# Performance work log

Measured on AMD Instinct MI355X. Metric: run time of the kernel, lower is better.

## Reference

```python
import jax, jax.numpy as jnp
import numpy as np

NUM_PATCHES = 64
PATCH_DIM = 256
HIDDEN = 512
HEADS = 8
SEQ = 1 + NUM_PATCHES  # 65
OUT_DIM = 10
BLOCKS = 6


def _ln2d(x, w, b):
    # LayerNorm over last two dims (seq, hidden), eps=1e-5, affine shape (SEQ, HIDDEN)
    mu = jnp.mean(x, axis=(-2, -1), keepdims=True)
    var = jnp.var(x, axis=(-2, -1), keepdims=True)
    return (x - mu) / jnp.sqrt(var + 1e-5) * w + b


def setup_inputs() -> dict:
    key = jax.random.key(0)
    ks = jax.random.split(key, 22)
    s = 0.02
    inp = {
        'X': jax.random.normal(ks[0], (256, 1, 128, 128), jnp.float32),
        'Wp': jax.random.normal(ks[1], (PATCH_DIM, HIDDEN), jnp.float32) * s,
        'bp': jnp.zeros((HIDDEN,), jnp.float32),
        'cls': jax.random.uniform(ks[2], (1, HIDDEN), jnp.float32),
        'pos': jax.random.uniform(ks[3], (SEQ, HIDDEN), jnp.float32),
        'ln1_w': jnp.ones((SEQ, HIDDEN), jnp.float32),
        'ln1_b': jnp.zeros((SEQ, HIDDEN), jnp.float32),
        'Wq': jax.random.normal(ks[4], (HEADS, HIDDEN, HIDDEN), jnp.float32) * s,
        'bq': jnp.zeros((HEADS, HIDDEN), jnp.float32),
        'Wk': jax.random.normal(ks[5], (HEADS, HIDDEN, HIDDEN), jnp.float32) * s,
        'bk': jnp.zeros((HEADS, HIDDEN), jnp.float32),
        'Wv': jax.random.normal(ks[6], (HEADS, HIDDEN, HIDDEN), jnp.float32) * s,
        'bv': jnp.zeros((HEADS, HIDDEN), jnp.float32),
        'Wo': jax.random.normal(ks[7], (HEADS * HIDDEN, HIDDEN), jnp.float32) * s,
        'bo': jnp.zeros((HIDDEN,), jnp.float32),
        'ln2_w': jnp.ones((SEQ, HIDDEN), jnp.float32),
        'ln2_b': jnp.zeros((SEQ, HIDDEN), jnp.float32),
        'W2': jax.random.normal(ks[8], (HIDDEN, HIDDEN), jnp.float32) * s,
        'b2': jnp.zeros((HIDDEN,), jnp.float32),
        'Wh': jax.random.normal(ks[9], (HIDDEN, OUT_DIM), jnp.float32) * s,
        'bh': jnp.zeros((OUT_DIM,), jnp.float32),
    }
    return inp


def reference(X, Wp, bp, cls, pos, ln1_w, ln1_b, Wq, bq, Wk, bk, Wv, bv, Wo, bo, ln2_w, ln2_b, W2, b2, Wh, bh):
    N = X.shape[0]
    patches = X.reshape(N, NUM_PATCHES, PATCH_DIM)
    E = patches @ Wp + bp                              # [N, 64, 512]
    E = jnp.concatenate([jnp.broadcast_to(cls, (N, 1, HIDDEN)), E], axis=1)
    Z = E + pos                                        # [N, 65, 512]
    scale = 1.0 / float(HIDDEN) ** 2                   # note: /hidden_dim**2 as in source
    for _ in range(BLOCKS):  # SAME weights reused each block (shared modules)
        Zn = _ln2d(Z, ln1_w, ln1_b)
        q = jnp.einsum('nsd,hde->nhse', Zn, Wq) + bq[None, :, None, :]
        k = jnp.einsum('nsd,hde->nhse', Zn, Wk) + bk[None, :, None, :]
        v = jnp.einsum('nsd,hde->nhse', Zn, Wv) + bv[None, :, None, :]
        attn = jax.nn.softmax(jnp.einsum('nhse,nhte->nhst', q, k) * scale, axis=-1)
        h = jnp.einsum('nhst,nhte->nhse', attn, v)     # [N, H, S, D]
        Hcat = jnp.transpose(h, (0, 2, 1, 3)).reshape(N, SEQ, HEADS * HIDDEN)
        res1 = Hcat @ Wo + bo                          # [N, 65, 512]
        Z = _ln2d(res1 + Z, ln2_w, ln2_b) @ W2 + b2    # no residual after this (as in source)
    return jnp.tanh(Z[:, 0] @ Wh + bh)
```

## Files before the change

kernel.cpp:

```cpp
#include <hip/hip_runtime.h>


typedef unsigned short u16;
typedef __attribute__((ext_vector_type(8))) short s8v;
typedef __attribute__((ext_vector_type(4))) float f4v;

#define MFMA16(a, b, c) __builtin_amdgcn_mfma_f32_16x16x32_bf16((a), (b), (c), 0, 0, 0)

__device__ __forceinline__ u16 f2bf(float f) {
    union { float f; unsigned int u; } c; c.f = f;
    unsigned int u = c.u;
    return (u16)((u + 0x7FFFu + ((u >> 16) & 1u)) >> 16);
}
__device__ __forceinline__ unsigned int pack2(float a, float b) {
    return (unsigned int)f2bf(a) | ((unsigned int)f2bf(b) << 16);
}
__device__ __forceinline__ float bflo(unsigned int u) {
    union { unsigned int i; float f; } c; c.i = u << 16; return c.f;
}
__device__ __forceinline__ float bfhi(unsigned int u) {
    union { unsigned int i; float f; } c; c.i = u & 0xffff0000u; return c.f;
}

__global__ __launch_bounds__(256) void vit_prep1(
    const float* __restrict__ Wp, const float* __restrict__ W2,
    const float* __restrict__ Wo, const float* __restrict__ Wv,
    const float* __restrict__ w1, const float* __restrict__ b1,
    const float* __restrict__ ln2w, const float* __restrict__ ln2b,
    const float* __restrict__ bv,
    u16* __restrict__ WpT, u16* __restrict__ W2T, u16* __restrict__ WoT,
    u16* __restrict__ Ap, float* __restrict__ W1c, float* __restrict__ B1m,
    unsigned int* __restrict__ w1q, unsigned int* __restrict__ w1t,
    unsigned int* __restrict__ lnp, float* __restrict__ bep) {
    __shared__ float t[64][65];
    const int bid = blockIdx.x, tid = threadIdx.x;
    if (bid < 608) {
        const float* in; u16* out; int R, C, bx, by;
        if (bid < 32)      { in = Wp; out = WpT; R = 256;  C = 512; int l = bid;      bx = l & 3;  by = l >> 2; }
        else if (bid < 96) { in = W2; out = W2T; R = 512;  C = 512; int l = bid - 32; bx = l & 7;  by = l >> 3; }
        else               { in = Wo; out = WoT; R = 4096; C = 512; int l = bid - 96; bx = l & 63; by = l >> 6; }
        const int r0 = bx * 64, c0 = by * 64;
        const int lr = tid >> 6, lc = tid & 63;
#pragma unroll
        for (int i = 0; i < 16; ++i) {
            int rr = i * 4 + lr;
            t[rr][lc] = in[(long)(r0 + rr) * C + c0 + lc];
        }
        __syncthreads();
#pragma unroll
        for (int i = 0; i < 16; ++i) {
            int rr = i * 4 + lr;
            out[(long)(c0 + rr) * R + r0 + lc] = f2bf(t[lc][rr]);
        }
    } else if (bid < 1632) {
        int base = (bid - 608) * 2048 + tid;
#pragma unroll
        for (int q = 0; q < 8; ++q) {
            int o = base + q * 256;
            int d = o >> 12, he = o & 4095;
            int h = he >> 9, e = he & 511;
            Ap[o] = f2bf(Wv[((long)h << 18) + (d << 9) + e]);
        }
    } else if (bid < 1830) {
        int id = (bid - 1632) * 256 + tid;
        if (id < 512) {
            float sw = 0.f, sb = 0.f;
            for (int s = 0; s < 65; ++s) { sw += w1[s * 512 + id]; sb += b1[s * 512 + id]; }
            W1c[id] = sw; B1m[id] = sb * (1.f / 65.f);
        }
        int i1 = id - 512;
        if (i1 >= 0 && i1 < 16896) {
            int s2 = i1 >> 9, d = i1 & 511;
            float lo = w1[(2 * s2) * 512 + d];
            float hi = (2 * s2 + 1 < 65) ? w1[(2 * s2 + 1) * 512 + d] : 0.f;
            unsigned int pk = pack2(lo, hi);
            if (s2 < 32) w1q[(s2 >> 2) * 2048 + d * 4 + (s2 & 3)] = pk;
            else         w1t[d] = pk;
        }
        int i2 = id - 17408;
        if (i2 >= 0 && i2 < 33280) {
            lnp[i2] = ((unsigned int)f2bf(ln2w[i2]) << 16) | (unsigned int)f2bf(ln2b[i2]);
        }
    } else {
        int z = bid - 1830;
#pragma unroll
        for (int jj = 0; jj < 2; ++jj) {
            int j = tid + jj * 256;
            float a = 0.f;
            for (int he = z * 32; he < z * 32 + 32; ++he)
                a += bv[he] * Wo[(long)he * 512 + j];
            bep[z * 512 + j] = a;
        }
    }
}

__global__ __launch_bounds__(512) void vit_prep2(
    const float* __restrict__ Wpart, const float* __restrict__ bep,
    const float* __restrict__ bo, unsigned int* __restrict__ Weffp,
    float* __restrict__ beff) {
    const int bid = blockIdx.x, tid = threadIdx.x;
    if (bid < 256) {
        int id = bid * 512 + tid;
        int kk = id >> 9, j = id & 511;
        float lo = 0.f, hi = 0.f;
#pragma unroll 4
        for (int z = 0; z < 32; ++z) {
            lo += Wpart[(long)z * 262144 + (2 * kk) * 512 + j];
            hi += Wpart[(long)z * 262144 + (2 * kk + 1) * 512 + j];
        }
        Weffp[(kk >> 2) * 2048 + j * 4 + (kk & 3)] = pack2(lo, hi);
    } else {
        float a = bo[tid];
        for (int z = 0; z < 128; ++z) a += bep[z * 512 + tid];
        beff[tid] = a;
    }
}

template<int K>
__global__ __launch_bounds__(512) void vit_gemmB(
    const u16* __restrict__ A, const u16* __restrict__ BT,
    float* __restrict__ out, int Arow, int Brow) {
    constexpr int BROW = K + 8;
    __shared__ __align__(16) u16 Bs[128 * BROW];
    const int tid = threadIdx.x, w = tid >> 6, lane = tid & 63;
    const int ml = lane & 15, kh = lane >> 4;
    const int m0 = blockIdx.x * 256, n0 = blockIdx.y * 128, k0 = blockIdx.z * K;
    out += (long)blockIdx.z * 262144;

    constexpr int CH = K / 8;
    for (int idx = tid; idx < 128 * CH; idx += 512) {
        int r = idx / CH, c = idx - r * CH;
        *(uint4*)&Bs[r * BROW + c * 8] =
            *(const uint4*)(BT + (long)(n0 + r) * Brow + k0 + c * 8);
    }
    __syncthreads();

    const u16* Abase = A + (long)(m0 + w * 32 + ml) * Arow + k0 + kh * 8;
    const long Astep16 = (long)16 * Arow;

    f4v acc[2][8];
#pragma unroll
    for (int mt = 0; mt < 2; ++mt)
#pragma unroll
        for (int j = 0; j < 8; ++j) acc[mt][j] = (f4v){0.f, 0.f, 0.f, 0.f};

    constexpr int NSTEP = K / 32;
    s8v a_cur[2], a_nxt[2];
    a_cur[0] = *(const s8v*)(Abase);
    a_cur[1] = *(const s8v*)(Abase + Astep16);
#pragma unroll
    for (int s = 0; s < NSTEP; ++s) {
        if (s + 1 < NSTEP) {
            a_nxt[0] = *(const s8v*)(Abase + (s + 1) * 32);
            a_nxt[1] = *(const s8v*)(Abase + Astep16 + (s + 1) * 32);
        }
#pragma unroll
        for (int j = 0; j < 8; ++j) {
            s8v b = *(const s8v*)&Bs[(j * 16 + ml) * BROW + s * 32 + kh * 8];
            acc[0][j] = MFMA16(a_cur[0], b, acc[0][j]);
            acc[1][j] = MFMA16(a_cur[1], b, acc[1][j]);
        }
        a_cur[0] = a_nxt[0]; a_cur[1] = a_nxt[1];
    }

#pragma unroll
    for (int mt = 0; mt < 2; ++mt)
#pragma unroll
        for (int j = 0; j < 8; ++j) {
            int n_g = n0 + j * 16 + ml;
#pragma unroll
            for (int r = 0; r < 4; ++r) {
                int m_g = m0 + w * 32 + mt * 16 + kh * 4 + r;
                out[(long)m_g * 512 + n_g] = acc[mt][j][r];
            }
        }
}

__global__ __launch_bounds__(512) void vit_fused(
    const float* __restrict__ X, const u16* __restrict__ WpT,
    const float* __restrict__ bp, const float* __restrict__ cls,
    const float* __restrict__ pos,
    const float* __restrict__ W1c, const float* __restrict__ B1m,
    const unsigned int* __restrict__ w1q, const unsigned int* __restrict__ w1t,
    const unsigned int* __restrict__ Weffp, const float* __restrict__ beff,
    const unsigned int* __restrict__ lnp,
    const u16* __restrict__ W2T, const float* __restrict__ b2,
    const float* __restrict__ Wh, const float* __restrict__ bh,
    float* __restrict__ out) {
    __shared__ __align__(16) char blob[139392];
    float* ZL   = (float*)blob;
    float* RmL  = (float*)(blob + 133120);
    float* ZnmL = (float*)(blob + 135168);
    float* csL  = (float*)(blob + 137216);
    float* red  = (float*)(blob + 139264);
    const float4* Rm4 = (const float4*)RmL;

    const int n = blockIdx.x, tid = threadIdx.x;
    const int w = tid >> 6, lane = tid & 63;
    const int ml = lane & 15, kh = lane >> 4;

    {
        const float* xf = X + (long)n * 16384;
        f4v eacc[4][4];
#pragma unroll
        for (int mt = 0; mt < 4; ++mt)
#pragma unroll
            for (int j = 0; j < 4; ++j) eacc[mt][j] = (f4v){0.f, 0.f, 0.f, 0.f};
#pragma unroll 1
        for (int st = 0; st < 8; ++st) {
            s8v b[4];
#pragma unroll
            for (int j = 0; j < 4; ++j)
                b[j] = *(const s8v*)(WpT + (long)(w * 64 + j * 16 + ml) * 256 +
                                     st * 32 + kh * 8);
#pragma unroll
            for (int mt = 0; mt < 4; ++mt) {
                const float* ap = xf + (mt * 16 + ml) * 256 + st * 32 + kh * 8;
                float4 xa = *(const float4*)ap;
                float4 xb = *(const float4*)(ap + 4);
                union { s8v v; u16 h[8]; } au;
                au.h[0] = f2bf(xa.x); au.h[1] = f2bf(xa.y);
                au.h[2] = f2bf(xa.z); au.h[3] = f2bf(xa.w);
                au.h[4] = f2bf(xb.x); au.h[5] = f2bf(xb.y);
                au.h[6] = f2bf(xb.z); au.h[7] = f2bf(xb.w);
#pragma unroll
                for (int j = 0; j < 4; ++j) eacc[mt][j] = MFMA16(au.v, b[j], eacc[mt][j]);
            }
        }
        float se = 0.f, sse = 0.f;
        float v0 = cls[tid] + pos[tid];
        ZL[tid] = v0; se += v0; sse += v0 * v0;
#pragma unroll
        for (int mt = 0; mt < 4; ++mt)
#pragma unroll
            for (int j = 0; j < 4; ++j) {
                int col = w * 64 + j * 16 + ml;
                float bpv = bp[col];
#pragma unroll
                for (int r = 0; r < 4; ++r) {
                    int zrow = mt * 16 + kh * 4 + r + 1;
                    float v = eacc[mt][j][r] + bpv + pos[zrow * 512 + col];
                    ZL[zrow * 512 + col] = v;
                    se += v; sse += v * v;
                }
            }
        for (int off = 32; off > 0; off >>= 1) {
            se += __shfl_down(se, off); sse += __shfl_down(sse, off);
        }
        if (lane == 0) { red[w] = se; red[8 + w] = sse; }
    }
    __syncthreads();

#pragma unroll 1
    for (int blk = 0; blk < 6; ++blk) {
        float S = 0.f, SS = 0.f;
#pragma unroll
        for (int i = 0; i < 8; ++i) { S += red[i]; SS += red[8 + i]; }
        const float mu = S * (1.f / 33280.f);
        const float r1 = rsqrtf(SS * (1.f / 33280.f) - mu * mu + 1e-5f);

        {
            float sw = 0.f, cs = 0.f;
            const uint4* W1Q = (const uint4*)w1q;
#pragma unroll 2
            for (int g = 0; g < 8; ++g) {
                uint4 u = W1Q[g * 512 + tid];
                int s0 = g * 8;
                float z0 = ZL[(s0 + 0) * 512 + tid], z1 = ZL[(s0 + 1) * 512 + tid];
                float z2 = ZL[(s0 + 2) * 512 + tid], z3 = ZL[(s0 + 3) * 512 + tid];
                float z4 = ZL[(s0 + 4) * 512 + tid], z5 = ZL[(s0 + 5) * 512 + tid];
                float z6 = ZL[(s0 + 6) * 512 + tid], z7 = ZL[(s0 + 7) * 512 + tid];
                cs += z0 + z1 + z2 + z3 + z4 + z5 + z6 + z7;
                sw += z0 * bflo(u.x) + z1 * bfhi(u.x);
                sw += z2 * bflo(u.y) + z3 * bfhi(u.y);
                sw += z4 * bflo(u.z) + z5 * bfhi(u.z);
                sw += z6 * bflo(u.w) + z7 * bfhi(u.w);
            }
            float zt = ZL[64 * 512 + tid];
            cs += zt;
            sw += zt * bflo(w1t[tid]);
            ZnmL[tid] = r1 * ((sw - mu * W1c[tid]) * (1.f / 65.f)) + B1m[tid];
            csL[tid] = cs;
        }
        __syncthreads();

        float mu2, r2;
        {
            const uint4* W4 = (const uint4*)Weffp;
            float a0 = 0.f, a1 = 0.f, a2 = 0.f, a3 = 0.f;
#pragma unroll 4
            for (int g = 0; g < 64; ++g) {
                uint4 u = W4[g * 512 + tid];
                int k0 = g * 8;
                a0 += ZnmL[k0 + 0] * bflo(u.x) + ZnmL[k0 + 1] * bfhi(u.x);
                a1 += ZnmL[k0 + 2] * bflo(u.y) + ZnmL[k0 + 3] * bfhi(u.y);
                a2 += ZnmL[k0 + 4] * bflo(u.z) + ZnmL[k0 + 5] * bfhi(u.z);
                a3 += ZnmL[k0 + 6] * bflo(u.w) + ZnmL[k0 + 7] * bfhi(u.w);
            }
            float rm = a0 + a1 + a2 + a3 + beff[tid];
            RmL[tid] = rm;
            float p1 = rm, p2 = rm * rm, p3 = rm * csL[tid];
            for (int off = 32; off > 0; off >>= 1) {
                p1 += __shfl_down(p1, off);
                p2 += __shfl_down(p2, off);
                p3 += __shfl_down(p3, off);
            }
            if (lane == 0) { red[w] = p1; red[8 + w] = p2; red[16 + w] = p3; }
            __syncthreads();
            float SR = 0.f, SR2 = 0.f, SRC = 0.f;
#pragma unroll
            for (int i = 0; i < 8; ++i) {
                SR += red[i]; SR2 += red[8 + i]; SRC += red[16 + i];
            }
            float S2 = S + 65.f * SR;
            float SS2 = SS + 2.f * SRC + 65.f * SR2;
            mu2 = S2 * (1.f / 33280.f);
            r2 = rsqrtf(SS2 * (1.f / 33280.f) - mu2 * mu2 + 1e-5f);
        }

#pragma unroll 1
        for (int it = 0; it < 9; ++it) {
            int row = it * 8 + w;
            if (row < 65) {
                const float* zr = ZL + row * 512;
                float4 z0 = *(const float4*)(zr + lane * 8);
                float4 z1 = *(const float4*)(zr + lane * 8 + 4);
                uint4 l0 = *(const uint4*)(lnp + row * 512 + lane * 8);
                uint4 l1 = *(const uint4*)(lnp + row * 512 + lane * 8 + 4);
                float4 rm0 = Rm4[lane * 2], rm1 = Rm4[lane * 2 + 1];
                float o0 = ((z0.x + rm0.x) - mu2) * r2 * bfhi(l0.x) + bflo(l0.x);
                float o1 = ((z0.y + rm0.y) - mu2) * r2 * bfhi(l0.y) + bflo(l0.y);
                float o2 = ((z0.z + rm0.z) - mu2) * r2 * bfhi(l0.z) + bflo(l0.z);
                float o3 = ((z0.w + rm0.w) - mu2) * r2 * bfhi(l0.w) + bflo(l0.w);
                float o4 = ((z1.x + rm1.x) - mu2) * r2 * bfhi(l1.x) + bflo(l1.x);
                float o5 = ((z1.y + rm1.y) - mu2) * r2 * bfhi(l1.y) + bflo(l1.y);
                float o6 = ((z1.z + rm1.z) - mu2) * r2 * bfhi(l1.z) + bflo(l1.z);
                float o7 = ((z1.w + rm1.w) - mu2) * r2 * bfhi(l1.w) + bflo(l1.w);
                uint4 pk;
                pk.x = pack2(o0, o1); pk.y = pack2(o2, o3);
                pk.z = pack2(o4, o5); pk.w = pack2(o6, o7);
                *(uint4*)(blob + row * 2064 + lane * 16) = pk;
            }
        }
        __syncthreads();

        int arow[5];
#pragma unroll
        for (int mt = 0; mt < 5; ++mt) {
            int rr = mt * 16 + ml;
            arow[mt] = (rr > 64) ? 64 : rr;
        }
        f4v acc[5][4];
#pragma unroll
        for (int mt = 0; mt < 5; ++mt)
#pragma unroll
            for (int j = 0; j < 4; ++j) acc[mt][j] = (f4v){0.f, 0.f, 0.f, 0.f};
        {
            s8v bcur[4], bnxt[4];
#pragma unroll
            for (int j = 0; j < 4; ++j)
                bcur[j] = *(const s8v*)(W2T + (long)(w * 64 + j * 16 + ml) * 512 + kh * 8);
#pragma unroll 1
            for (int st = 0; st < 16; ++st) {
                if (st < 15) {
#pragma unroll
                    for (int j = 0; j < 4; ++j)
                        bnxt[j] = *(const s8v*)(W2T + (long)(w * 64 + j * 16 + ml) * 512 +
                                                (st + 1) * 32 + kh * 8);
                }
#pragma unroll
                for (int mt = 0; mt < 5; ++mt) {
                    s8v a = *(const s8v*)(blob + arow[mt] * 2064 + st * 64 + kh * 16);
#pragma unroll
                    for (int j = 0; j < 4; ++j) acc[mt][j] = MFMA16(a, bcur[j], acc[mt][j]);
                }
#pragma unroll
                for (int j = 0; j < 4; ++j) bcur[j] = bnxt[j];
            }
        }
        __syncthreads();

        if (blk < 5) {
            float sn = 0.f, ssn = 0.f;
#pragma unroll
            for (int mt = 0; mt < 5; ++mt)
#pragma unroll
                for (int j = 0; j < 4; ++j) {
                    int col = w * 64 + j * 16 + ml;
                    float bbv = b2[col];
#pragma unroll
                    for (int r = 0; r < 4; ++r) {
                        int row = mt * 16 + kh * 4 + r;
                        if (row < 65) {
                            float v = acc[mt][j][r] + bbv;
                            ZL[row * 512 + col] = v;
                            sn += v; ssn += v * v;
                        }
                    }
                }
            for (int off = 32; off > 0; off >>= 1) {
                sn += __shfl_down(sn, off); ssn += __shfl_down(ssn, off);
            }
            if (lane == 0) { red[w] = sn; red[8 + w] = ssn; }
            __syncthreads();
        } else {
            if (kh == 0) {
#pragma unroll
                for (int j = 0; j < 4; ++j) {
                    int col = w * 64 + j * 16 + ml;
                    RmL[col] = acc[0][j][0] + b2[col];
                }
            }
            __syncthreads();
            if (tid < 64) {
                float a10[10];
#pragma unroll
                for (int jj = 0; jj < 10; ++jj) a10[jj] = 0.f;
#pragma unroll
                for (int i = 0; i < 8; ++i) {
                    int k = tid * 8 + i;
                    float zv = RmL[k];
#pragma unroll
                    for (int jj = 0; jj < 10; ++jj) a10[jj] += zv * Wh[k * 10 + jj];
                }
                for (int off = 32; off > 0; off >>= 1) {
#pragma unroll
                    for (int jj = 0; jj < 10; ++jj) a10[jj] += __shfl_down(a10[jj], off);
                }
                if (tid == 0) {
#pragma unroll
                    for (int jj = 0; jj < 10; ++jj)
                        out[n * 10 + jj] = tanhf(a10[jj] + bh[jj]);
                }
            }
        }
    }
}

static const size_t OFF_WPT   = 0;
static const size_t OFF_W2T   = 262144;
static const size_t OFF_WOT   = 786432;
static const size_t OFF_AP    = 4980736;
static const size_t OFF_WEFFP = 9175040;
static const size_t OFF_WPART = 9699328;
static const size_t OFF_BEP   = 43253760;
static const size_t OFF_BEFF  = 43515904;
static const size_t OFF_W1C   = 43517952;
static const size_t OFF_B1M   = 43520000;
static const size_t OFF_W1Q   = 43522048;
static const size_t OFF_W1T   = 43587584;
static const size_t OFF_LNP   = 43589632;

extern "C" void kernel_launch(void* const* d_in, const int* in_sizes, int n_in,
                              void* d_out, int out_size, void* d_ws, size_t ws_size,
                              hipStream_t stream) {
    const float* X    = (const float*)d_in[0];
    const float* Wp   = (const float*)d_in[1];
    const float* bp   = (const float*)d_in[2];
    const float* cls  = (const float*)d_in[3];
    const float* pos  = (const float*)d_in[4];
    const float* ln1w = (const float*)d_in[5];
    const float* ln1b = (const float*)d_in[6];
    const float* Wv   = (const float*)d_in[11];
    const float* bv   = (const float*)d_in[12];
    const float* Wo   = (const float*)d_in[13];
    const float* bo   = (const float*)d_in[14];
    const float* ln2w = (const float*)d_in[15];
    const float* ln2b = (const float*)d_in[16];
    const float* W2   = (const float*)d_in[17];
    const float* b2   = (const float*)d_in[18];
    const float* Wh   = (const float*)d_in[19];
    const float* bh   = (const float*)d_in[20];

    char* ws = (char*)d_ws;
    u16* WpT     = (u16*)(ws + OFF_WPT);
    u16* W2T     = (u16*)(ws + OFF_W2T);
    u16* WoT     = (u16*)(ws + OFF_WOT);
    u16* Ap      = (u16*)(ws + OFF_AP);
    unsigned int* Weffp = (unsigned int*)(ws + OFF_WEFFP);
    float* Wpart = (float*)(ws + OFF_WPART);
    float* bep   = (float*)(ws + OFF_BEP);
    float* beff  = (float*)(ws + OFF_BEFF);
    float* W1c   = (float*)(ws + OFF_W1C);
    float* B1m   = (float*)(ws + OFF_B1M);
    unsigned int* w1q = (unsigned int*)(ws + OFF_W1Q);
    unsigned int* w1t = (unsigned int*)(ws + OFF_W1T);
    unsigned int* lnp = (unsigned int*)(ws + OFF_LNP);

    vit_prep1<<<dim3(1958), dim3(256), 0, stream>>>(
        Wp, W2, Wo, Wv, ln1w, ln1b, ln2w, ln2b, bv,
        WpT, W2T, WoT, Ap, W1c, B1m, w1q, w1t, lnp, bep);
    vit_gemmB<128><<<dim3(2, 4, 32), dim3(512), 0, stream>>>(
        Ap, WoT, Wpart, 4096, 4096);
    vit_prep2<<<dim3(257), dim3(512), 0, stream>>>(Wpart, bep, bo, Weffp, beff);

    vit_fused<<<dim3(256), dim3(512), 0, stream>>>(
        X, WpT, bp, cls, pos, W1c, B1m, w1q, w1t, Weffp, beff, lnp, W2T, b2,
        Wh, bh, (float*)d_out);
}
```

Measured before the change: 333.3 us.

## Double fused kernel block to 1024 threads and split reductions across halves

The fused ViT kernel now launches 1024 threads per block instead of 512. The column-sum and Weff matvec stages split their reduction dimension between two thread halves and combine partials through new shared buffers, and the MFMA GEMMs give each wave 32 columns instead of 64. The aim is more waves per CU to hide latency in this one-block-per-sample kernel, since only 256 blocks run. In exchange it adds extra syncthreads and partial-sum passes, grows shared memory use, and tightens the register budget under launch_bounds(1024).

```diff
diff --git a/kernel.cpp b/kernel.cpp
--- a/kernel.cpp
+++ b/kernel.cpp
@@ -176,7 +176,7 @@
         }
 }
 
-__global__ __launch_bounds__(512) void vit_fused(
+__global__ __launch_bounds__(1024) void vit_fused(
     const float* __restrict__ X, const u16* __restrict__ WpT,
     const float* __restrict__ bp, const float* __restrict__ cls,
     const float* __restrict__ pos,
@@ -187,31 +187,33 @@
     const u16* __restrict__ W2T, const float* __restrict__ b2,
     const float* __restrict__ Wh, const float* __restrict__ bh,
     float* __restrict__ out) {
-    __shared__ __align__(16) char blob[139392];
+    __shared__ __align__(16) char blob[145600];
     float* ZL   = (float*)blob;
     float* RmL  = (float*)(blob + 133120);
     float* ZnmL = (float*)(blob + 135168);
-    float* csL  = (float*)(blob + 137216);
-    float* red  = (float*)(blob + 139264);
+    float* swP  = (float*)(blob + 137216);
+    float* csP  = (float*)(blob + 141312);
+    float* red  = (float*)(blob + 145408);
     const float4* Rm4 = (const float4*)RmL;
 
     const int n = blockIdx.x, tid = threadIdx.x;
     const int w = tid >> 6, lane = tid & 63;
     const int ml = lane & 15, kh = lane >> 4;
+    const int j0 = w * 32;
 
     {
         const float* xf = X + (long)n * 16384;
-        f4v eacc[4][4];
+        f4v eacc[4][2];
 #pragma unroll
         for (int mt = 0; mt < 4; ++mt)
 #pragma unroll
-            for (int j = 0; j < 4; ++j) eacc[mt][j] = (f4v){0.f, 0.f, 0.f, 0.f};
+            for (int j = 0; j < 2; ++j) eacc[mt][j] = (f4v){0.f, 0.f, 0.f, 0.f};
 #pragma unroll 1
         for (int st = 0; st < 8; ++st) {
-            s8v b[4];
-#pragma unroll
-            for (int j = 0; j < 4; ++j)
-                b[j] = *(const s8v*)(WpT + (long)(w * 64 + j * 16 + ml) * 256 +
+            s8v b[2];
+#pragma unroll
+            for (int j = 0; j < 2; ++j)
+                b[j] = *(const s8v*)(WpT + (long)(j0 + j * 16 + ml) * 256 +
                                      st * 32 + kh * 8);
 #pragma unroll
             for (int mt = 0; mt < 4; ++mt) {
@@ -224,17 +226,19 @@
                 au.h[4] = f2bf(xb.x); au.h[5] = f2bf(xb.y);
                 au.h[6] = f2bf(xb.z); au.h[7] = f2bf(xb.w);
 #pragma unroll
-                for (int j = 0; j < 4; ++j) eacc[mt][j] = MFMA16(au.v, b[j], eacc[mt][j]);
+                for (int j = 0; j < 2; ++j) eacc[mt][j] = MFMA16(au.v, b[j], eacc[mt][j]);
             }
         }
         float se = 0.f, sse = 0.f;
-        float v0 = cls[tid] + pos[tid];
-        ZL[tid] = v0; se += v0; sse += v0 * v0;
+        if (tid < 512) {
+            float v0 = cls[tid] + pos[tid];
+            ZL[tid] = v0; se += v0; sse += v0 * v0;
+        }
 #pragma unroll
         for (int mt = 0; mt < 4; ++mt)
 #pragma unroll
-            for (int j = 0; j < 4; ++j) {
-                int col = w * 64 + j * 16 + ml;
+            for (int j = 0; j < 2; ++j) {
+                int col = j0 + j * 16 + ml;
                 float bpv = bp[col];
 #pragma unroll
                 for (int r = 0; r < 4; ++r) {
@@ -247,7 +251,7 @@
         for (int off = 32; off > 0; off >>= 1) {
             se += __shfl_down(se, off); sse += __shfl_down(sse, off);
         }
-        if (lane == 0) { red[w] = se; red[8 + w] = sse; }
+        if (lane == 0) { red[w] = se; red[16 + w] = sse; }
     }
     __syncthreads();
 
@@ -255,62 +259,81 @@
     for (int blk = 0; blk < 6; ++blk) {
         float S = 0.f, SS = 0.f;
 #pragma unroll
-        for (int i = 0; i < 8; ++i) { S += red[i]; SS += red[8 + i]; }
+        for (int i = 0; i < 16; ++i) { S += red[i]; SS += red[16 + i]; }
         const float mu = S * (1.f / 33280.f);
         const float r1 = rsqrtf(SS * (1.f / 33280.f) - mu * mu + 1e-5f);
 
         {
+            const int d = tid & 511, h2 = tid >> 9;
+            const uint4* W1Q = (const uint4*)w1q;
             float sw = 0.f, cs = 0.f;
-            const uint4* W1Q = (const uint4*)w1q;
-#pragma unroll 2
-            for (int g = 0; g < 8; ++g) {
-                uint4 u = W1Q[g * 512 + tid];
+            const int g0 = h2 * 4;
+#pragma unroll
+            for (int gg = 0; gg < 4; ++gg) {
+                int g = g0 + gg;
+                uint4 u = W1Q[g * 512 + d];
                 int s0 = g * 8;
-                float z0 = ZL[(s0 + 0) * 512 + tid], z1 = ZL[(s0 + 1) * 512 + tid];
-                float z2 = ZL[(s0 + 2) * 512 + tid], z3 = ZL[(s0 + 3) * 512 + tid];
-                float z4 = ZL[(s0 + 4) * 512 + tid], z5 = ZL[(s0 + 5) * 512 + tid];
-                float z6 = ZL[(s0 + 6) * 512 + tid], z7 = ZL[(s0 + 7) * 512 + tid];
+                float z0 = ZL[(s0 + 0) * 512 + d], z1 = ZL[(s0 + 1) * 512 + d];
+                float z2 = ZL[(s0 + 2) * 512 + d], z3 = ZL[(s0 + 3) * 512 + d];
+                float z4 = ZL[(s0 + 4) * 512 + d], z5 = ZL[(s0 + 5) * 512 + d];
+                float z6 = ZL[(s0 + 6) * 512 + d], z7 = ZL[(s0 + 7) * 512 + d];
                 cs += z0 + z1 + z2 + z3 + z4 + z5 + z6 + z7;
                 sw += z0 * bflo(u.x) + z1 * bfhi(u.x);
                 sw += z2 * bflo(u.y) + z3 * bfhi(u.y);
                 sw += z4 * bflo(u.z) + z5 * bfhi(u.z);
                 sw += z6 * bflo(u.w) + z7 * bfhi(u.w);
             }
-            float zt = ZL[64 * 512 + tid];
-            cs += zt;
-            sw += zt * bflo(w1t[tid]);
+            if (h2) {
+                float zt = ZL[64 * 512 + d];
+                cs += zt; sw += zt * bflo(w1t[d]);
+            }
+            swP[h2 * 512 + d] = sw; csP[h2 * 512 + d] = cs;
+        }
+        __syncthreads();
+        if (tid < 512) {
+            float sw = swP[tid] + swP[512 + tid];
+            float cs = csP[tid] + csP[512 + tid];
             ZnmL[tid] = r1 * ((sw - mu * W1c[tid]) * (1.f / 65.f)) + B1m[tid];
-            csL[tid] = cs;
+            csP[tid] = cs;
         }
         __syncthreads();
 
-        float mu2, r2;
         {
+            const int j = tid & 511, h2 = tid >> 9;
             const uint4* W4 = (const uint4*)Weffp;
             float a0 = 0.f, a1 = 0.f, a2 = 0.f, a3 = 0.f;
+            const int ge = h2 * 32;
 #pragma unroll 4
-            for (int g = 0; g < 64; ++g) {
-                uint4 u = W4[g * 512 + tid];
+            for (int gg = 0; gg < 32; ++gg) {
+                int g = ge + gg;
+                uint4 u = W4[g * 512 + j];
                 int k0 = g * 8;
                 a0 += ZnmL[k0 + 0] * bflo(u.x) + ZnmL[k0 + 1] * bfhi(u.x);
                 a1 += ZnmL[k0 + 2] * bflo(u.y) + ZnmL[k0 + 3] * bfhi(u.y);
                 a2 += ZnmL[k0 + 4] * bflo(u.z) + ZnmL[k0 + 5] * bfhi(u.z);
                 a3 += ZnmL[k0 + 6] * bflo(u.w) + ZnmL[k0 + 7] * bfhi(u.w);
             }
-            float rm = a0 + a1 + a2 + a3 + beff[tid];
-            RmL[tid] = rm;
-            float p1 = rm, p2 = rm * rm, p3 = rm * csL[tid];
-            for (int off = 32; off > 0; off >>= 1) {
-                p1 += __shfl_down(p1, off);
-                p2 += __shfl_down(p2, off);
-                p3 += __shfl_down(p3, off);
-            }
-            if (lane == 0) { red[w] = p1; red[8 + w] = p2; red[16 + w] = p3; }
+            swP[h2 * 512 + j] = a0 + a1 + a2 + a3;
+        }
+        __syncthreads();
+        float mu2, r2;
+        {
+            if (tid < 512) {
+                float rm = swP[tid] + swP[512 + tid] + beff[tid];
+                RmL[tid] = rm;
+                float p1 = rm, p2 = rm * rm, p3 = rm * csP[tid];
+                for (int off = 32; off > 0; off >>= 1) {
+                    p1 += __shfl_down(p1, off);
+                    p2 += __shfl_down(p2, off);
+                    p3 += __shfl_down(p3, off);
+                }
+                if (lane == 0) { red[w] = p1; red[16 + w] = p2; red[32 + w] = p3; }
+            }
             __syncthreads();
             float SR = 0.f, SR2 = 0.f, SRC = 0.f;
 #pragma unroll
             for (int i = 0; i < 8; ++i) {
-                SR += red[i]; SR2 += red[8 + i]; SRC += red[16 + i];
+                SR += red[i]; SR2 += red[16 + i]; SRC += red[32 + i];
             }
             float S2 = S + 65.f * SR;
             float SS2 = SS + 2.f * SRC + 65.f * SR2;
@@ -319,8 +342,8 @@
         }
 
 #pragma unroll 1
-        for (int it = 0; it < 9; ++it) {
-            int row = it * 8 + w;
+        for (int it = 0; it < 5; ++it) {
+            int row = it * 16 + w;
             if (row < 65) {
                 const float* zr = ZL + row * 512;
                 float4 z0 = *(const float4*)(zr + lane * 8);
@@ -350,32 +373,32 @@
             int rr = mt * 16 + ml;
             arow[mt] = (rr > 64) ? 64 : rr;
         }
-        f4v acc[5][4];
+        f4v acc[5][2];
 #pragma unroll
         for (int mt = 0; mt < 5; ++mt)
 #pragma unroll
-            for (int j = 0; j < 4; ++j) acc[mt][j] = (f4v){0.f, 0.f, 0.f, 0.f};
+            for (int j = 0; j < 2; ++j) acc[mt][j] = (f4v){0.f, 0.f, 0.f, 0.f};
         {
-            s8v bcur[4], bnxt[4];
-#pragma unroll
-            for (int j = 0; j < 4; ++j)
-                bcur[j] = *(const s8v*)(W2T + (long)(w * 64 + j * 16 + ml) * 512 + kh * 8);
+            s8v bcur[2], bnxt[2];
+#pragma unroll
+            for (int j = 0; j < 2; ++j)
+                bcur[j] = *(const s8v*)(W2T + (long)(j0 + j * 16 + ml) * 512 + kh * 8);
 #pragma unroll 1
             for (int st = 0; st < 16; ++st) {
                 if (st < 15) {
 #pragma unroll
-                    for (int j = 0; j < 4; ++j)
-                        bnxt[j] = *(const s8v*)(W2T + (long)(w * 64 + j * 16 + ml) * 512 +
+                    for (int j = 0; j < 2; ++j)
+                        bnxt[j] = *(const s8v*)(W2T + (long)(j0 + j * 16 + ml) * 512 +
                                                 (st + 1) * 32 + kh * 8);
                 }
 #pragma unroll
                 for (int mt = 0; mt < 5; ++mt) {
                     s8v a = *(const s8v*)(blob + arow[mt] * 2064 + st * 64 + kh * 16);
 #pragma unroll
-                    for (int j = 0; j < 4; ++j) acc[mt][j] = MFMA16(a, bcur[j], acc[mt][j]);
-                }
-#pragma unroll
-                for (int j = 0; j < 4; ++j) bcur[j] = bnxt[j];
+                    for (int j = 0; j < 2; ++j) acc[mt][j] = MFMA16(a, bcur[j], acc[mt][j]);
+                }
+#pragma unroll
+                for (int j = 0; j < 2; ++j) bcur[j] = bnxt[j];
             }
         }
         __syncthreads();
@@ -385,8 +408,8 @@
 #pragma unroll
             for (int mt = 0; mt < 5; ++mt)
 #pragma unroll
-                for (int j = 0; j < 4; ++j) {
-                    int col = w * 64 + j * 16 + ml;
+                for (int j = 0; j < 2; ++j) {
+                    int col = j0 + j * 16 + ml;
                     float bbv = b2[col];
 #pragma unroll
                     for (int r = 0; r < 4; ++r) {
@@ -401,13 +424,13 @@
             for (int off = 32; off > 0; off >>= 1) {
                 sn += __shfl_down(sn, off); ssn += __shfl_down(ssn, off);
             }
-            if (lane == 0) { red[w] = sn; red[8 + w] = ssn; }
+            if (lane == 0) { red[w] = sn; red[16 + w] = ssn; }
             __syncthreads();
         } else {
             if (kh == 0) {
 #pragma unroll
-                for (int j = 0; j < 4; ++j) {
-                    int col = w * 64 + j * 16 + ml;
+                for (int j = 0; j < 2; ++j) {
+                    int col = j0 + j * 16 + ml;
                     RmL[col] = acc[0][j][0] + b2[col];
                 }
             }
@@ -494,7 +517,7 @@
         Ap, WoT, Wpart, 4096, 4096);
     vit_prep2<<<dim3(257), dim3(512), 0, stream>>>(Wpart, bep, bo, Weffp, beff);
 
-    vit_fused<<<dim3(256), dim3(512), 0, stream>>>(
+    vit_fused<<<dim3(256), dim3(1024), 0, stream>>>(
         X, WpT, bp, cls, pos, W1c, B1m, w1q, w1t, Weffp, beff, lnp, W2T, b2,
         Wh, bh, (float*)d_out);
 }
```

New measurement: 459.2 us. 1.38x slower.
